# Kernel optimization log

Measured on AMD Instinct MI355X. Metric: run time of the kernel, lower is better.

The kernel has to match this reference:

```python
import jax, jax.numpy as jnp
import numpy as np

B, T, N, F = 4, 1, 12500, 64
C = 64        # spatial_hidden_dim (heads=1)
OUT = 64      # spatial_out_features
E = 1600000
NT = B * N    # total flattened nodes


def setup_inputs() -> dict:
    key = jax.random.key(0)
    ks = jax.random.split(key, 12)
    s = lambda d: 1.0 / np.sqrt(d)
    return {
        "x": jax.random.normal(ks[0], (B, T, N, F), jnp.float32),
        "edge_index": jax.random.randint(ks[1], (2, E), 0, NT, jnp.int64),
        "edge_attr": jax.random.uniform(ks[2], (E, 1), jnp.float32),
        "W_l": jax.random.normal(ks[3], (F, C), jnp.float32) * s(F),
        "b_l": jnp.zeros((C,), jnp.float32),
        "W_r": jax.random.normal(ks[4], (F, C), jnp.float32) * s(F),
        "b_r": jnp.zeros((C,), jnp.float32),
        "W_e": jax.random.normal(ks[5], (1, C), jnp.float32),
        "att": jax.random.normal(ks[6], (C,), jnp.float32) * s(C),
        "bias": jnp.zeros((C,), jnp.float32),
        "W_fc": jax.random.normal(ks[7], (C, OUT), jnp.float32) * s(C),
        "b_fc": jnp.zeros((OUT,), jnp.float32),
    }


def reference(x, edge_index, edge_attr, W_l, b_l, W_r, b_r, W_e, att, bias, W_fc, b_fc):
    Bx, Tx, Nx, Fx = x.shape
    x2 = x.reshape(Bx * Nx, Fx)                      # [NT, F] (requires T==1)
    xl = x2 @ W_l + b_l                              # [NT, C] source transform
    xr = x2 @ W_r + b_r                              # [NT, C] target transform
    src, dst = edge_index[0], edge_index[1]
    e = edge_attr @ W_e                              # [E, C] lin_edge (no bias)
    m = jax.nn.leaky_relu(xl[src] + xr[dst] + e, 0.2)  # [E, C]
    score = m @ att                                  # [E]
    # segment softmax over destination nodes
    smax = jax.lax.stop_gradient(jax.ops.segment_max(score, dst, num_segments=Bx * Nx))
    ex = jnp.exp(score - smax[dst])
    denom = jax.ops.segment_sum(ex, dst, num_segments=Bx * Nx)
    alpha = ex / denom[dst]                          # [E]
    agg = jax.ops.segment_sum(alpha[:, None] * xl[src], dst, num_segments=Bx * Nx)
    out = (agg + bias).reshape(Bx, Nx, -1)           # [B, N, C]
    return out @ W_fc + b_fc                         # [B, N, OUT]
```

## Files before the change

kernel.cpp:

```cpp
#include <hip/hip_runtime.h>
#include <math.h>

#define LRELU(v) ((v) >= 0.f ? (v) : 0.2f * (v))

#define NB_SHIFT 4
#define BKT_NODES 16
#define MAXB 768
#define MAX_NBKT 3200
#define BIN_CHUNK 16384
#define TR_BLOCKS 512
#define EAQ_INV (1.0f / 4095.0f)

__device__ __forceinline__ unsigned short f32_to_bf16_rne(float f) {
    unsigned int b = __float_as_uint(f);
    b += 0x7FFFu + ((b >> 16) & 1u);
    return (unsigned short)(b >> 16);
}
__device__ __forceinline__ unsigned int pack_bf16x2(float lo, float hi) {
    return (unsigned int)f32_to_bf16_rne(lo) | ((unsigned int)f32_to_bf16_rne(hi) << 16);
}
__device__ __forceinline__ unsigned int mk_pkt(int src, int dst, float eav) {
    int q = (int)(eav * 4095.f + 0.5f);
    q = q < 0 ? 0 : (q > 4095 ? 4095 : q);
    return (unsigned int)src | ((unsigned int)(dst & (BKT_NODES - 1)) << 16)
         | ((unsigned int)q << 20);
}

__global__ void __launch_bounds__(256) k_prep(
    const float* __restrict__ x,
    const float* __restrict__ W_l, const float* __restrict__ b_l,
    const float* __restrict__ W_r, const float* __restrict__ b_r,
    unsigned short* __restrict__ xl16, float* __restrict__ xr,
    const int* __restrict__ ei, const float* __restrict__ ea,
    int* __restrict__ bcnt, unsigned int* __restrict__ bucket,
    int NT, int E, int nbkt, int binBlocks)
{
    __shared__ __align__(16) char smem[33792];
    const int t = threadIdx.x;
    if ((int)blockIdx.x < binBlocks) {
        int* lh = (int*)smem;
        int* lb = lh + MAX_NBKT;
        const int e0 = (int)blockIdx.x * BIN_CHUNK;
        const int e1 = (e0 + BIN_CHUNK < E) ? e0 + BIN_CHUNK : E;
        const int n = e1 - e0;
        const int nv4 = n >> 2;
        const int4* d4 = (const int4*)(ei + E + e0);
        const int4* s4 = (const int4*)(ei + e0);
        const float4* a4 = (const float4*)(ea + e0);
        for (int i = t; i < nbkt; i += 256) lh[i] = 0;
        __syncthreads();
        for (int j = t; j < nv4; j += 256) {
            const int4 v = d4[j];
            atomicAdd(&lh[v.x >> NB_SHIFT], 1);
            atomicAdd(&lh[v.y >> NB_SHIFT], 1);
            atomicAdd(&lh[v.z >> NB_SHIFT], 1);
            atomicAdd(&lh[v.w >> NB_SHIFT], 1);
        }
        for (int j = e0 + (nv4 << 2) + t; j < e1; j += 256)
            atomicAdd(&lh[ei[E + j] >> NB_SHIFT], 1);
        __syncthreads();
        for (int i = t; i < nbkt; i += 256) {
            const int c = lh[i];
            lb[i] = c ? atomicAdd(&bcnt[i], c) : 0;
            lh[i] = 0;
        }
        __syncthreads();
        for (int j = t; j < nv4; j += 256) {
            const int4 dv = d4[j];
            const int4 sv = s4[j];
            const float4 av = a4[j];
            int bkt, pos;
            bkt = dv.x >> NB_SHIFT;
            pos = lb[bkt] + atomicAdd(&lh[bkt], 1);
            if (pos < MAXB) bucket[(size_t)bkt * MAXB + pos] = mk_pkt(sv.x, dv.x, av.x);
            bkt = dv.y >> NB_SHIFT;
            pos = lb[bkt] + atomicAdd(&lh[bkt], 1);
            if (pos < MAXB) bucket[(size_t)bkt * MAXB + pos] = mk_pkt(sv.y, dv.y, av.y);
            bkt = dv.z >> NB_SHIFT;
            pos = lb[bkt] + atomicAdd(&lh[bkt], 1);
            if (pos < MAXB) bucket[(size_t)bkt * MAXB + pos] = mk_pkt(sv.z, dv.z, av.z);
            bkt = dv.w >> NB_SHIFT;
            pos = lb[bkt] + atomicAdd(&lh[bkt], 1);
            if (pos < MAXB) bucket[(size_t)bkt * MAXB + pos] = mk_pkt(sv.w, dv.w, av.w);
        }
        for (int j = e0 + (nv4 << 2) + t; j < e1; j += 256) {
            const int dst = ei[E + j];
            const int bkt = dst >> NB_SHIFT;
            const int pos = lb[bkt] + atomicAdd(&lh[bkt], 1);
            if (pos < MAXB)
                bucket[(size_t)bkt * MAXB + pos] = mk_pkt(ei[j], dst, ea[j]);
        }
    } else {
        float* sWl = (float*)smem;
        float* sWr = sWl + 64 * 64;
        float* sx  = sWr + 64 * 64;
        for (int i = t; i < 64 * 64; i += 256) { sWl[i] = W_l[i]; sWr[i] = W_r[i]; }
        const float bl = b_l[t & 63];
        const float br = b_r[t & 63];
        const int nTiles = (NT + 3) / 4;
        const int ln = t & 63;
        const int nr = t >> 6;
        for (int tile = (int)blockIdx.x - binBlocks; tile < nTiles; tile += TR_BLOCKS) {
            __syncthreads();
            const int node0 = tile * 4;
            if (node0 * 64 + t < NT * 64) sx[t] = x[node0 * 64 + t];
            __syncthreads();
            const int node = node0 + nr;
            if (node < NT) {
                float sl = bl, sr = br;
                #pragma unroll
                for (int k = 0; k < 64; ++k) {
                    const float xv = sx[nr * 64 + k];
                    sl = fmaf(xv, sWl[k * 64 + ln], sl);
                    sr = fmaf(xv, sWr[k * 64 + ln], sr);
                }
                xl16[node * 64 + ln] = f32_to_bf16_rne(sl);
                xr[node * 64 + ln] = sr;
            }
        }
    }
}

__global__ void __launch_bounds__(256) k_fused(
    const int* __restrict__ bcnt, const unsigned int* __restrict__ bucket,
    const unsigned short* __restrict__ xl16, const float* __restrict__ xr,
    const float* __restrict__ W_e, const float* __restrict__ att,
    const float* __restrict__ bias, unsigned short* __restrict__ agg16, int NT)
{
    __shared__ unsigned short perm16[MAXB];
    __shared__ int hist[BKT_NODES], base[BKT_NODES], cur[BKT_NODES];
    const int t = threadIdx.x;
    const int lane = t & 63;
    const int w = t >> 6;
    const int hl = lane & 7;
    const int h = lane >> 3;
    const int b = blockIdx.x;
    const unsigned int* gb = bucket + (size_t)b * MAXB;
    int cnt = bcnt[b];
    if (cnt > MAXB) cnt = MAXB;

    if (t < BKT_NODES) hist[t] = 0;
    __syncthreads();
    for (int i = t; i < cnt; i += 256)
        atomicAdd(&hist[(gb[i] >> 16) & (BKT_NODES - 1)], 1);
    __syncthreads();
    if (t == 0) {
        int run = 0;
        #pragma unroll
        for (int l = 0; l < BKT_NODES; ++l) { base[l] = run; cur[l] = run; run += hist[l]; }
    }
    __syncthreads();
    for (int i = t; i < cnt; i += 256) {
        const int dl = (gb[i] >> 16) & (BKT_NODES - 1);
        perm16[atomicAdd(&cur[dl], 1)] = (unsigned short)i;
    }
    __syncthreads();

    const float4 we0 = ((const float4*)W_e)[2 * hl];
    const float4 we1 = ((const float4*)W_e)[2 * hl + 1];
    const float4 at0 = ((const float4*)att)[2 * hl];
    const float4 at1 = ((const float4*)att)[2 * hl + 1];
    const float4 bv0 = ((const float4*)bias)[2 * hl];
    const float4 bv1 = ((const float4*)bias)[2 * hl + 1];

    #pragma unroll
    for (int k = 0; k < 4; ++k) {
        const int l = w * 4 + k;
        const int node = b * BKT_NODES + l;
        if (node >= NT) break;
        const int sbeg = base[l];
        const int scnt = hist[l];
        const float4 xr0 = ((const float4*)xr)[node * 16 + 2 * hl];
        const float4 xr1 = ((const float4*)xr)[node * 16 + 2 * hl + 1];
        float a0 = 0.f, a1 = 0.f, a2 = 0.f, a3 = 0.f;
        float a4 = 0.f, a5 = 0.f, a6 = 0.f, a7 = 0.f;
        float den = 0.f;
        for (int c0 = 0; c0 < scnt; c0 += 64) {
            const int i = c0 + lane;
            unsigned int my = 0u;
            if (i < scnt) my = gb[perm16[sbeg + i]];
            const int cc = (scnt - c0 < 64) ? scnt - c0 : 64;
            for (int tt = 0; tt < cc; tt += 8) {
                const int eidx = tt + h;
                const unsigned int pk = (unsigned int)__shfl((int)my, eidx);
                const int srcl = pk & 0xFFFF;
                const float eav = (float)(pk >> 20) * EAQ_INV;
                const bool act = eidx < cc;
                float x0 = 0.f, x1 = 0.f, x2 = 0.f, x3 = 0.f;
                float x4 = 0.f, x5 = 0.f, x6 = 0.f, x7 = 0.f;
                if (act) {
                    const uint4 xb = ((const uint4*)(xl16 + (size_t)srcl * 64))[hl];
                    x0 = __uint_as_float(xb.x << 16);
                    x1 = __uint_as_float(xb.x & 0xFFFF0000u);
                    x2 = __uint_as_float(xb.y << 16);
                    x3 = __uint_as_float(xb.y & 0xFFFF0000u);
                    x4 = __uint_as_float(xb.z << 16);
                    x5 = __uint_as_float(xb.z & 0xFFFF0000u);
                    x6 = __uint_as_float(xb.w << 16);
                    x7 = __uint_as_float(xb.w & 0xFFFF0000u);
                }
                float v0 = x0 + xr0.x + eav * we0.x;
                float v1 = x1 + xr0.y + eav * we0.y;
                float v2 = x2 + xr0.z + eav * we0.z;
                float v3 = x3 + xr0.w + eav * we0.w;
                float v4 = x4 + xr1.x + eav * we1.x;
                float v5 = x5 + xr1.y + eav * we1.y;
                float v6 = x6 + xr1.z + eav * we1.z;
                float v7 = x7 + xr1.w + eav * we1.w;
                v0 = LRELU(v0); v1 = LRELU(v1); v2 = LRELU(v2); v3 = LRELU(v3);
                v4 = LRELU(v4); v5 = LRELU(v5); v6 = LRELU(v6); v7 = LRELU(v7);
                float p = v0 * at0.x + v1 * at0.y + v2 * at0.z + v3 * at0.w
                        + v4 * at1.x + v5 * at1.y + v6 * at1.z + v7 * at1.w;
                p += __shfl_xor(p, 1);
                p += __shfl_xor(p, 2);
                p += __shfl_xor(p, 4);
                const float ex = act ? __expf(p) : 0.f;
                den += ex;
                a0 = fmaf(ex, x0, a0); a1 = fmaf(ex, x1, a1);
                a2 = fmaf(ex, x2, a2); a3 = fmaf(ex, x3, a3);
                a4 = fmaf(ex, x4, a4); a5 = fmaf(ex, x5, a5);
                a6 = fmaf(ex, x6, a6); a7 = fmaf(ex, x7, a7);
            }
        }
        #pragma unroll
        for (int o = 8; o < 64; o <<= 1) {
            a0 += __shfl_xor(a0, o); a1 += __shfl_xor(a1, o);
            a2 += __shfl_xor(a2, o); a3 += __shfl_xor(a3, o);
            a4 += __shfl_xor(a4, o); a5 += __shfl_xor(a5, o);
            a6 += __shfl_xor(a6, o); a7 += __shfl_xor(a7, o);
            den += __shfl_xor(den, o);
        }
        const float inv = (den > 0.f) ? 1.f / den : 0.f;
        if (h == 0) {
            uint4 r;
            r.x = pack_bf16x2(fmaf(a0, inv, bv0.x), fmaf(a1, inv, bv0.y));
            r.y = pack_bf16x2(fmaf(a2, inv, bv0.z), fmaf(a3, inv, bv0.w));
            r.z = pack_bf16x2(fmaf(a4, inv, bv1.x), fmaf(a5, inv, bv1.y));
            r.w = pack_bf16x2(fmaf(a6, inv, bv1.z), fmaf(a7, inv, bv1.w));
            ((uint4*)(agg16 + (size_t)node * 64))[hl] = r;
        }
    }
}

__global__ void __launch_bounds__(256) k_out(
    const unsigned short* __restrict__ agg16,
    const float* __restrict__ W_fc, const float* __restrict__ b_fc,
    float* __restrict__ out, int NT)
{
    __shared__ float sW[64 * 64];
    __shared__ float sa[4 * 64];
    const int t = threadIdx.x;
    for (int i = t; i < 64 * 64; i += 256) sW[i] = W_fc[i];
    const int node0 = blockIdx.x * 4;
    if (t < 128 && node0 * 64 + 2 * t < NT * 64) {
        const unsigned int v = ((const unsigned int*)agg16)[node0 * 32 + t];
        sa[2 * t]     = __uint_as_float(v << 16);
        sa[2 * t + 1] = __uint_as_float(v & 0xFFFF0000u);
    }
    __syncthreads();
    const int ln = t & 63;
    const int nr = t >> 6;
    const int node = node0 + nr;
    if (node < NT) {
        float s = b_fc[ln];
        #pragma unroll
        for (int k = 0; k < 64; ++k) s = fmaf(sa[nr * 64 + k], sW[k * 64 + ln], s);
        out[node * 64 + ln] = s;
    }
}

extern "C" void kernel_launch(void* const* d_in, const int* in_sizes, int n_in,
                              void* d_out, int out_size, void* d_ws, size_t ws_size,
                              hipStream_t stream) {
    const float* x    = (const float*)d_in[0];
    const int*   ei   = (const int*)d_in[1];
    const float* ea   = (const float*)d_in[2];
    const float* W_l  = (const float*)d_in[3];
    const float* b_l  = (const float*)d_in[4];
    const float* W_r  = (const float*)d_in[5];
    const float* b_r  = (const float*)d_in[6];
    const float* W_e  = (const float*)d_in[7];
    const float* att  = (const float*)d_in[8];
    const float* bias = (const float*)d_in[9];
    const float* W_fc = (const float*)d_in[10];
    const float* b_fc = (const float*)d_in[11];
    float* out = (float*)d_out;

    const int NT = in_sizes[0] / 64;
    const int E  = in_sizes[2];
    const int nbkt = (NT + BKT_NODES - 1) / BKT_NODES;

    unsigned short* xl16 = (unsigned short*)d_ws;
    float* xr    = (float*)(xl16 + (size_t)NT * 64);
    unsigned short* agg16 = (unsigned short*)(xr + (size_t)NT * 64);
    unsigned int* bucket = (unsigned int*)(agg16 + (size_t)NT * 64);
    int* bcnt    = (int*)(bucket + (size_t)nbkt * MAXB);

    const int binBlocks = (E + BIN_CHUNK - 1) / BIN_CHUNK;
    const int nodeBlocks = (NT + 3) / 4;

    hipMemsetAsync(bcnt, 0, (size_t)nbkt * sizeof(int), stream);
    k_prep<<<binBlocks + TR_BLOCKS, 256, 0, stream>>>(
        x, W_l, b_l, W_r, b_r, xl16, xr, ei, ea, bcnt, bucket,
        NT, E, nbkt, binBlocks);
    k_fused<<<nbkt, 256, 0, stream>>>(bcnt, bucket, xl16, xr, W_e, att,
                                      bias, agg16, NT);
    k_out<<<nodeBlocks, 256, 0, stream>>>(agg16, W_fc, b_fc, out, NT);
}
```

Measured before the change: 142.3 us.

## Split edge binning into coarse and fine two-pass radix scatter

Edge bucketing by destination now runs in two passes. The first pass scatters edges into about 49 coarse buckets of 1024 nodes as 8-byte packets. A new kernel then re-bins each coarse bucket into the 16-node fine buckets. This replaces a large shared histogram and thousands of scattered global atomics and writes per chunk with far fewer coarse ones. The cost is an extra kernel launch and an extra round trip of roughly 12.8 MB through memory.

```diff
diff --git a/kernel.cpp b/kernel.cpp
--- a/kernel.cpp
+++ b/kernel.cpp
@@ -6,7 +6,10 @@
 #define NB_SHIFT 4
 #define BKT_NODES 16
 #define MAXB 768
-#define MAX_NBKT 3200
+#define MAX_NBKT 3136
+#define CB_SHIFT 10
+#define MAXC 34304
+#define MAX_NC 64
 #define BIN_CHUNK 16384
 #define TR_BLOCKS 512
 #define EAQ_INV (1.0f / 4095.0f)
@@ -32,14 +35,14 @@
     const float* __restrict__ W_r, const float* __restrict__ b_r,
     unsigned short* __restrict__ xl16, float* __restrict__ xr,
     const int* __restrict__ ei, const float* __restrict__ ea,
-    int* __restrict__ bcnt, unsigned int* __restrict__ bucket,
-    int NT, int E, int nbkt, int binBlocks)
+    int* __restrict__ ccnt, uint2* __restrict__ coarse,
+    int NT, int E, int nc, int binBlocks)
 {
     __shared__ __align__(16) char smem[33792];
     const int t = threadIdx.x;
     if ((int)blockIdx.x < binBlocks) {
         int* lh = (int*)smem;
-        int* lb = lh + MAX_NBKT;
+        int* lb = lh + MAX_NC;
         const int e0 = (int)blockIdx.x * BIN_CHUNK;
         const int e1 = (e0 + BIN_CHUNK < E) ? e0 + BIN_CHUNK : E;
         const int n = e1 - e0;
@@ -47,48 +50,58 @@
         const int4* d4 = (const int4*)(ei + E + e0);
         const int4* s4 = (const int4*)(ei + e0);
         const float4* a4 = (const float4*)(ea + e0);
-        for (int i = t; i < nbkt; i += 256) lh[i] = 0;
+        if (t < nc) lh[t] = 0;
         __syncthreads();
         for (int j = t; j < nv4; j += 256) {
             const int4 v = d4[j];
-            atomicAdd(&lh[v.x >> NB_SHIFT], 1);
-            atomicAdd(&lh[v.y >> NB_SHIFT], 1);
-            atomicAdd(&lh[v.z >> NB_SHIFT], 1);
-            atomicAdd(&lh[v.w >> NB_SHIFT], 1);
+            atomicAdd(&lh[v.x >> CB_SHIFT], 1);
+            atomicAdd(&lh[v.y >> CB_SHIFT], 1);
+            atomicAdd(&lh[v.z >> CB_SHIFT], 1);
+            atomicAdd(&lh[v.w >> CB_SHIFT], 1);
         }
         for (int j = e0 + (nv4 << 2) + t; j < e1; j += 256)
-            atomicAdd(&lh[ei[E + j] >> NB_SHIFT], 1);
+            atomicAdd(&lh[ei[E + j] >> CB_SHIFT], 1);
         __syncthreads();
-        for (int i = t; i < nbkt; i += 256) {
-            const int c = lh[i];
-            lb[i] = c ? atomicAdd(&bcnt[i], c) : 0;
-            lh[i] = 0;
+        if (t < nc) {
+            const int c = lh[t];
+            lb[t] = c ? atomicAdd(&ccnt[t], c) : 0;
+            lh[t] = 0;
         }
         __syncthreads();
         for (int j = t; j < nv4; j += 256) {
             const int4 dv = d4[j];
             const int4 sv = s4[j];
             const float4 av = a4[j];
-            int bkt, pos;
-            bkt = dv.x >> NB_SHIFT;
-            pos = lb[bkt] + atomicAdd(&lh[bkt], 1);
-            if (pos < MAXB) bucket[(size_t)bkt * MAXB + pos] = mk_pkt(sv.x, dv.x, av.x);
-            bkt = dv.y >> NB_SHIFT;
-            pos = lb[bkt] + atomicAdd(&lh[bkt], 1);
-            if (pos < MAXB) bucket[(size_t)bkt * MAXB + pos] = mk_pkt(sv.y, dv.y, av.y);
-            bkt = dv.z >> NB_SHIFT;
-            pos = lb[bkt] + atomicAdd(&lh[bkt], 1);
-            if (pos < MAXB) bucket[(size_t)bkt * MAXB + pos] = mk_pkt(sv.z, dv.z, av.z);
-            bkt = dv.w >> NB_SHIFT;
-            pos = lb[bkt] + atomicAdd(&lh[bkt], 1);
-            if (pos < MAXB) bucket[(size_t)bkt * MAXB + pos] = mk_pkt(sv.w, dv.w, av.w);
+            int cb, pos;
+            cb = dv.x >> CB_SHIFT;
+            pos = lb[cb] + atomicAdd(&lh[cb], 1);
+            if (pos < MAXC) coarse[(size_t)cb * MAXC + pos] =
+                make_uint2(__float_as_uint(av.x),
+                           (unsigned int)sv.x | ((unsigned int)(dv.x & 1023) << 16));
+            cb = dv.y >> CB_SHIFT;
+            pos = lb[cb] + atomicAdd(&lh[cb], 1);
+            if (pos < MAXC) coarse[(size_t)cb * MAXC + pos] =
+                make_uint2(__float_as_uint(av.y),
+                           (unsigned int)sv.y | ((unsigned int)(dv.y & 1023) << 16));
+            cb = dv.z >> CB_SHIFT;
+            pos = lb[cb] + atomicAdd(&lh[cb], 1);
+            if (pos < MAXC) coarse[(size_t)cb * MAXC + pos] =
+                make_uint2(__float_as_uint(av.z),
+                           (unsigned int)sv.z | ((unsigned int)(dv.z & 1023) << 16));
+            cb = dv.w >> CB_SHIFT;
+            pos = lb[cb] + atomicAdd(&lh[cb], 1);
+            if (pos < MAXC) coarse[(size_t)cb * MAXC + pos] =
+                make_uint2(__float_as_uint(av.w),
+                           (unsigned int)sv.w | ((unsigned int)(dv.w & 1023) << 16));
         }
         for (int j = e0 + (nv4 << 2) + t; j < e1; j += 256) {
             const int dst = ei[E + j];
-            const int bkt = dst >> NB_SHIFT;
-            const int pos = lb[bkt] + atomicAdd(&lh[bkt], 1);
-            if (pos < MAXB)
-                bucket[(size_t)bkt * MAXB + pos] = mk_pkt(ei[j], dst, ea[j]);
+            const int cb = dst >> CB_SHIFT;
+            const int pos = lb[cb] + atomicAdd(&lh[cb], 1);
+            if (pos < MAXC)
+                coarse[(size_t)cb * MAXC + pos] =
+                    make_uint2(__float_as_uint(ea[j]),
+                               (unsigned int)ei[j] | ((unsigned int)(dst & 1023) << 16));
         }
     } else {
         float* sWl = (float*)smem;
@@ -118,6 +131,44 @@
                 xr[node * 64 + ln] = sr;
             }
         }
+    }
+}
+
+__global__ void __launch_bounds__(256) k_bin2(
+    const int* __restrict__ ccnt, const uint2* __restrict__ coarse,
+    int* __restrict__ bcnt, unsigned int* __restrict__ bucket, int NT)
+{
+    __shared__ int lh[64], lb[64];
+    const int t = threadIdx.x;
+    const int cb = blockIdx.x >> 2;
+    const int q = blockIdx.x & 3;
+    int cnt = ccnt[cb];
+    if (cnt > MAXC) cnt = MAXC;
+    const int chunk = (cnt + 3) >> 2;
+    const int p0 = q * chunk;
+    const int p1 = (p0 + chunk < cnt) ? p0 + chunk : cnt;
+    const uint2* gc = coarse + (size_t)cb * MAXC;
+    const int fbase = cb << (CB_SHIFT - NB_SHIFT);
+
+    if (t < 64) lh[t] = 0;
+    __syncthreads();
+    for (int i = p0 + t; i < p1; i += 256)
+        atomicAdd(&lh[(gc[i].y >> 16) >> NB_SHIFT], 1);
+    __syncthreads();
+    if (t < 64) {
+        const int c = lh[t];
+        lb[t] = c ? atomicAdd(&bcnt[fbase + t], c) : 0;
+        lh[t] = 0;
+    }
+    __syncthreads();
+    for (int i = p0 + t; i < p1; i += 256) {
+        const uint2 pk = gc[i];
+        const int dstIn = pk.y >> 16;
+        const int f = dstIn >> NB_SHIFT;
+        const int pos = lb[f] + atomicAdd(&lh[f], 1);
+        if (pos < MAXB)
+            bucket[(size_t)(fbase + f) * MAXB + pos] =
+                mk_pkt((int)(pk.y & 0xFFFF), dstIn, __uint_as_float(pk.x));
     }
 }
 
@@ -289,20 +340,24 @@
     const int NT = in_sizes[0] / 64;
     const int E  = in_sizes[2];
     const int nbkt = (NT + BKT_NODES - 1) / BKT_NODES;
+    const int nc   = (NT + (1 << CB_SHIFT) - 1) >> CB_SHIFT;
 
     unsigned short* xl16 = (unsigned short*)d_ws;
     float* xr    = (float*)(xl16 + (size_t)NT * 64);
     unsigned short* agg16 = (unsigned short*)(xr + (size_t)NT * 64);
     unsigned int* bucket = (unsigned int*)(agg16 + (size_t)NT * 64);
-    int* bcnt    = (int*)(bucket + (size_t)nbkt * MAXB);
+    uint2* coarse = (uint2*)(bucket + (size_t)MAX_NBKT * MAXB);
+    int* bcnt    = (int*)(coarse + (size_t)nc * MAXC);
+    int* ccnt    = bcnt + MAX_NBKT;
 
     const int binBlocks = (E + BIN_CHUNK - 1) / BIN_CHUNK;
     const int nodeBlocks = (NT + 3) / 4;
 
-    hipMemsetAsync(bcnt, 0, (size_t)nbkt * sizeof(int), stream);
+    hipMemsetAsync(bcnt, 0, (size_t)(MAX_NBKT + MAX_NC) * sizeof(int), stream);
     k_prep<<<binBlocks + TR_BLOCKS, 256, 0, stream>>>(
-        x, W_l, b_l, W_r, b_r, xl16, xr, ei, ea, bcnt, bucket,
-        NT, E, nbkt, binBlocks);
+        x, W_l, b_l, W_r, b_r, xl16, xr, ei, ea, ccnt, coarse,
+        NT, E, nc, binBlocks);
+    k_bin2<<<nc * 4, 256, 0, stream>>>(ccnt, coarse, bcnt, bucket, NT);
     k_fused<<<nbkt, 256, 0, stream>>>(bcnt, bucket, xl16, xr, W_e, att,
                                       bias, agg16, NT);
     k_out<<<nodeBlocks, 256, 0, stream>>>(agg16, W_fc, b_fc, out, NT);
```

After: 161.4 us. 1.13x slower.
